# Kernel optimization log

Hardware: AMD Instinct MI355X
Metric: run time of the kernel (lower is better)

## Reference

```python
import jax, jax.numpy as jnp
import numpy as np

N_NODES = 100000
MAX_CHILD = 8
X_SIZE = 128
H_SIZE = 128
N_TYPES = 8
W_SCALE = 0.05  # keep gates out of saturation


def setup_inputs() -> dict:
    key = jax.random.key(0)
    ks = jax.random.split(key, 8)
    return {
        "x": jax.random.normal(ks[0], (N_NODES, X_SIZE), jnp.float32),
        "n_h": jax.random.normal(ks[1], (N_NODES, MAX_CHILD, H_SIZE), jnp.float32),
        "n_c": jax.random.normal(ks[2], (N_NODES, MAX_CHILD, H_SIZE), jnp.float32),
        "type_id": jax.random.randint(ks[3], (N_NODES,), 0, N_TYPES, jnp.int64),
        "W_iou": jax.random.normal(ks[4], (N_TYPES, X_SIZE, 3 * H_SIZE), jnp.float32) * W_SCALE,
        "U_iou": jax.random.normal(ks[5], (N_TYPES, H_SIZE, 3 * H_SIZE), jnp.float32) * W_SCALE,
        "b_iou": jnp.zeros((N_TYPES, 3 * H_SIZE), jnp.float32),
        "U_f": jax.random.normal(ks[6], (N_TYPES, H_SIZE, H_SIZE), jnp.float32) * W_SCALE,
        "b_f": jnp.zeros((N_TYPES, H_SIZE), jnp.float32),
    }


def reference(x, n_h, n_c, type_id, W_iou, U_iou, b_iou, U_f, b_f):
    # x: [N, X], n_h/n_c: [N, K, H] child mailbox, type_id: [N]
    N, K, H = n_h.shape
    T = W_iou.shape[0]
    h_sum = n_h.sum(axis=1)  # child-sum is linear -> aggregate before GEMM [N, H]

    # --- reduce_func: masked per-type child aggregation ---
    iou_aggr = jnp.zeros((N, 3 * H), x.dtype)
    c_aggr = jnp.zeros((N, H), x.dtype)
    for t in range(T):
        m = (type_id == t)[:, None]
        iou_t = h_sum @ U_iou[t]                                   # [N, 3H]
        f = jax.nn.sigmoid(jnp.einsum("nkh,hg->nkg", n_h, U_f[t]) + b_f[t])
        c_t = (f * n_c).sum(axis=1)                                # [N, H]
        iou_aggr = jnp.where(m, iou_t, iou_aggr)
        c_aggr = jnp.where(m, c_t, c_aggr)

    # --- apply_node_func: masked per-type node states ---
    h_out = jnp.zeros((N, H), x.dtype)
    c_out = jnp.zeros((N, H), x.dtype)
    for t in range(T):
        m = (type_id == t)[:, None]
        iou = x @ W_iou[t] + iou_aggr + b_iou[t]                   # [N, 3H]
        i_g, o_g, u_g = jnp.split(iou, 3, axis=1)
        c_t = jax.nn.sigmoid(i_g) * jnp.tanh(u_g) + c_aggr
        h_t = jax.nn.sigmoid(o_g) * jnp.tanh(c_t)
        h_out = jnp.where(m, h_t, h_out)
        c_out = jnp.where(m, c_t, c_out)
    return h_out, c_out
```

## Files before the change

kernel.cpp:

```cpp
#include <hip/hip_runtime.h>
#include <hip/hip_bf16.h>
#include <stdint.h>

typedef __bf16 bf16x8 __attribute__((ext_vector_type(8)));
typedef float  f32x4  __attribute__((ext_vector_type(4)));

#define H    128
#define KCH  8
#define NT   8
#define BM   32

#define WS_TILET  2048
#define WS_IDX    16384
#define WS_UF     458752
#define WS_W      720896

__device__ __forceinline__ float fsigm(float v){ return 1.f/(1.f+__expf(-v)); }
__device__ __forceinline__ float ftanh(float v){
  v = fminf(fmaxf(v,-15.f),15.f);
  float e = __expf(2.f*v);
  return (e-1.f)/(e+1.f);
}

__global__ void k_init(int* ws){ if (threadIdx.x < 40) ws[threadIdx.x] = 0; }

__global__ void k_detect(const int* __restrict__ type_id, int* ws){
  __shared__ int nz;
  if (threadIdx.x == 0) nz = 0;
  __syncthreads();
  int v = type_id[threadIdx.x];
  if ((threadIdx.x & 1) && v != 0) atomicAdd(&nz, 1);
  __syncthreads();
  if (threadIdx.x == 0) ws[25] = (nz == 0) ? 2 : 1;
}

__global__ void k_count(const int* __restrict__ type_id, int* __restrict__ ws, int N){
  __shared__ int h[NT];
  int tid = threadIdx.x;
  if (tid < NT) h[tid] = 0;
  __syncthreads();
  int stride = ws[25];
  int i = blockIdx.x*blockDim.x + tid;
  if (i < N) atomicAdd(&h[type_id[(size_t)i*stride]], 1);
  __syncthreads();
  if (tid < NT) atomicAdd(&ws[tid], h[tid]);
}

__global__ void k_scan(int* m){
  int s = 0;
  for (int t=0;t<NT;++t){
    m[16+t] = s;
    m[8+t]  = s;
    m[26+t] = s + m[t];
    s += ((m[t]+BM-1)/BM)*BM;
  }
  m[24] = s;
}

__global__ void k_scatter(const int* __restrict__ type_id, int* __restrict__ ws, int N){
  __shared__ int h[NT], base[NT];
  int tid = threadIdx.x;
  if (tid < NT) h[tid] = 0;
  __syncthreads();
  int stride = ws[25];
  int i = blockIdx.x*blockDim.x + tid;
  int t = 0, lp = 0;
  if (i < N){ t = type_id[(size_t)i*stride]; lp = atomicAdd(&h[t], 1); }
  __syncthreads();
  if (tid < NT) base[tid] = atomicAdd(&ws[8+tid], h[tid]);
  __syncthreads();
  if (i < N) ws[(WS_IDX/4) + base[t] + lp] = i;
}

__global__ void k_tiletype(int* ws, int ntiles){
  int i = blockIdx.x*256 + threadIdx.x;
  if (i >= ntiles) return;
  const int* op = ws + 16;
  int p = i*BM, t = -1;
  if (p < op[8]){
    for (int s=0;s<NT;++s) if (p >= op[s] && p < op[s+1]) t = s;
  }
  ws[(WS_TILET/4) + i] = t;
}

__global__ void k_prep_uf(const float* __restrict__ U_f, char* __restrict__ ws){
  int gid = blockIdx.x*256 + threadIdx.x;
  if (gid >= NT*128*16) return;
  int sp = gid & 15, c = (gid>>4) & 127, t = gid >> 11;
  int kbase = 8*(sp ^ (c & 7));
  const float* src = U_f + ((size_t)t*H + kbase)*H + c;
  bf16x8 v;
  #pragma unroll
  for (int j=0;j<8;++j) v[j] = (__bf16)src[(size_t)j*H];
  *(bf16x8*)(ws + WS_UF + (size_t)gid*16) = v;
}

__global__ void k_prep_w(const float* __restrict__ W_iou, const float* __restrict__ U_iou,
                         char* __restrict__ ws){
  int gid = blockIdx.x*256 + threadIdx.x;
  if (gid >= NT*384*32) return;
  int sp = gid & 31, col = (gid>>5) % 384, t = gid / (384*32);
  int K0 = sp*8;
  bf16x8 v;
  #pragma unroll
  for (int j=0;j<8;++j){
    int K = K0 + j;
    float f = (K < H) ? W_iou[((size_t)t*H + K)*(3*H) + col]
                      : U_iou[((size_t)t*H + (K-H))*(3*H) + col];
    v[j] = (__bf16)f;
  }
  *(bf16x8*)(ws + WS_W + (size_t)gid*16) = v;
}

__global__ __launch_bounds__(256,3) void k_phaseB(
  const float* __restrict__ n_h, const float* __restrict__ n_c,
  const float* __restrict__ b_f, const char* __restrict__ ws,
  float* __restrict__ out, int N)
{
  __shared__ __align__(16) char lds[49152];
  const int* meta = (const int*)ws;
  int tile = blockIdx.x;
  int t = ((const int*)(ws + WS_TILET))[tile];
  if (t < 0) return;
  int ev = meta[26 + t];
  const int* idx = (const int*)(ws + WS_IDX);

  int tid = threadIdx.x;
  int lane = tid & 63, wave = tid >> 6;
  int rw = wave & 1, cw = wave >> 1;
  int l15 = lane & 15, l4 = lane >> 4;
  int base = tile*BM;

  int mrow = tid >> 3, mcol = (tid & 7) * 16;
  int mpos = base + mrow;
  int mnode = (mpos < ev) ? idx[mpos] : 0;

  int npos = base + rw*16 + l15;
  bool valn = npos < ev;
  int nd = valn ? idx[npos] : 0;
  const float* ncb = n_c + (size_t)nd*(KCH*H);
  int ocb[4]; f32x4 bf4[4];
  #pragma unroll
  for (int st=0; st<4; ++st){
    ocb[st] = cw*64 + st*16 + 4*l4;
    bf4[st] = *(const f32x4*)(b_f + t*H + ocb[st]);
  }

  {
    const char* src = ws + WS_UF + (size_t)t*32768;
    #pragma unroll
    for (int it=0; it<8; ++it){
      bf16x8 v = *(const bf16x8*)(src + it*4096 + tid*16);
      *(bf16x8*)(lds + it*4096 + tid*16) = v;
    }
  }

  const float* nh_base = n_h + (size_t)mnode*(KCH*H) + mcol;

  float hsum[16];
  #pragma unroll
  for (int j=0;j<16;++j) hsum[j] = 0.f;
  f32x4 cacc[4];
  #pragma unroll
  for (int st=0;st<4;++st) cacc[st] = (f32x4){0.f,0.f,0.f,0.f};

  int arow = rw*16 + l15;
  int aswz = (arow & 7) << 4;
  int mswz = (mrow & 7) << 4;

  {
    const float4* p = (const float4*)nh_base;
    float4 a0=p[0], a1=p[1], a2=p[2], a3=p[3];
    hsum[0]+=a0.x;  hsum[1]+=a0.y;  hsum[2]+=a0.z;  hsum[3]+=a0.w;
    hsum[4]+=a1.x;  hsum[5]+=a1.y;  hsum[6]+=a1.z;  hsum[7]+=a1.w;
    hsum[8]+=a2.x;  hsum[9]+=a2.y;  hsum[10]+=a2.z; hsum[11]+=a2.w;
    hsum[12]+=a3.x; hsum[13]+=a3.y; hsum[14]+=a3.z; hsum[15]+=a3.w;
    bf16x8 w0, w1;
    w0[0]=(__bf16)a0.x; w0[1]=(__bf16)a0.y; w0[2]=(__bf16)a0.z; w0[3]=(__bf16)a0.w;
    w0[4]=(__bf16)a1.x; w0[5]=(__bf16)a1.y; w0[6]=(__bf16)a1.z; w0[7]=(__bf16)a1.w;
    w1[0]=(__bf16)a2.x; w1[1]=(__bf16)a2.y; w1[2]=(__bf16)a2.z; w1[3]=(__bf16)a2.w;
    w1[4]=(__bf16)a3.x; w1[5]=(__bf16)a3.y; w1[6]=(__bf16)a3.z; w1[7]=(__bf16)a3.w;
    *(bf16x8*)(lds + 32768 + mrow*256 + (( mcol*2      ) ^ mswz)) = w0;
    *(bf16x8*)(lds + 32768 + mrow*256 + (( mcol*2 + 16 ) ^ mswz)) = w1;
  }
  __syncthreads();

  #pragma unroll 1
  for (int k=0;k<KCH;++k){
    const int cur = 32768 + (k&1)*8192;
    const int nxt = 32768 + ((k+1)&1)*8192;
    float4 b0,b1,b2,b3;
    if (k < KCH-1){
      const float4* p = (const float4*)(nh_base + (size_t)(k+1)*H);
      b0=p[0]; b1=p[1]; b2=p[2]; b3=p[3];
    }
    f32x4 nc4[4];
    #pragma unroll
    for (int st=0;st<4;++st) nc4[st] = *(const f32x4*)(ncb + (size_t)k*H + ocb[st]);

    f32x4 fa[4];
    #pragma unroll
    for (int st=0;st<4;++st) fa[st] = (f32x4){0.f,0.f,0.f,0.f};
    #pragma unroll
    for (int kk=0; kk<4; ++kk){
      int kb = kk*64 + l4*16;
      bf16x8 bnh = *(const bf16x8*)(lds + cur + arow*256 + (kb ^ aswz));
      #pragma unroll
      for (int st=0;st<4;++st){
        int c = cw*64 + st*16 + l15;
        bf16x8 auf = *(const bf16x8*)(lds + c*256 + (kb ^ ((c&7)<<4)));
        fa[st] = __builtin_amdgcn_mfma_f32_16x16x32_bf16(auf, bnh, fa[st], 0,0,0);
      }
    }
    #pragma unroll
    for (int st=0;st<4;++st){
      #pragma unroll
      for (int r=0;r<4;++r){
        float fg = fsigm(fa[st][r] + bf4[st][r]);
        cacc[st][r] += fg * nc4[st][r];
      }
    }

    if (k < KCH-1){
      hsum[0]+=b0.x;  hsum[1]+=b0.y;  hsum[2]+=b0.z;  hsum[3]+=b0.w;
      hsum[4]+=b1.x;  hsum[5]+=b1.y;  hsum[6]+=b1.z;  hsum[7]+=b1.w;
      hsum[8]+=b2.x;  hsum[9]+=b2.y;  hsum[10]+=b2.z; hsum[11]+=b2.w;
      hsum[12]+=b3.x; hsum[13]+=b3.y; hsum[14]+=b3.z; hsum[15]+=b3.w;
      bf16x8 w0, w1;
      w0[0]=(__bf16)b0.x; w0[1]=(__bf16)b0.y; w0[2]=(__bf16)b0.z; w0[3]=(__bf16)b0.w;
      w0[4]=(__bf16)b1.x; w0[5]=(__bf16)b1.y; w0[6]=(__bf16)b1.z; w0[7]=(__bf16)b1.w;
      w1[0]=(__bf16)b2.x; w1[1]=(__bf16)b2.y; w1[2]=(__bf16)b2.z; w1[3]=(__bf16)b2.w;
      w1[4]=(__bf16)b3.x; w1[5]=(__bf16)b3.y; w1[6]=(__bf16)b3.z; w1[7]=(__bf16)b3.w;
      *(bf16x8*)(lds + nxt + mrow*256 + (( mcol*2      ) ^ mswz)) = w0;
      *(bf16x8*)(lds + nxt + mrow*256 + (( mcol*2 + 16 ) ^ mswz)) = w1;
    }
    __syncthreads();
  }

  if (mpos < ev){
    float4* dst = (float4*)(out + (size_t)mnode*H + mcol);
    dst[0] = make_float4(hsum[0], hsum[1], hsum[2], hsum[3]);
    dst[1] = make_float4(hsum[4], hsum[5], hsum[6], hsum[7]);
    dst[2] = make_float4(hsum[8], hsum[9], hsum[10],hsum[11]);
    dst[3] = make_float4(hsum[12],hsum[13],hsum[14],hsum[15]);
  }
  float* outc = out + (size_t)N*H;
  if (valn){
    #pragma unroll
    for (int st=0;st<4;++st)
      *(f32x4*)(outc + (size_t)nd*H + ocb[st]) = cacc[st];
  }
}

__global__ __launch_bounds__(256,4) void k_phaseA(
  const float* __restrict__ x, const float* __restrict__ b_iou,
  const char* __restrict__ ws, float* __restrict__ out, int N)
{
  __shared__ __align__(16) char lds[16384];
  const int* meta = (const int*)ws;
  int tile = blockIdx.x;
  int t = ((const int*)(ws + WS_TILET))[tile];
  if (t < 0) return;
  int ev = meta[26 + t];
  const int* idx = (const int*)(ws + WS_IDX);

  int tid = threadIdx.x;
  int lane = tid & 63, wave = tid >> 6;
  int rw = wave & 1, cw = wave >> 1;
  int l15 = lane & 15, l4 = lane >> 4;
  int base = tile*BM;

  int mrow = tid >> 3, mcol = (tid & 7) * 16;
  int mpos = base + mrow;
  int mnode = (mpos < ev) ? idx[mpos] : 0;

  int npos = base + rw*16 + l15;
  bool valn = npos < ev;
  int nd = valn ? idx[npos] : 0;

  int mswz = (mrow & 7) << 4;
  {
    const float4* px = (const float4*)(x   + (size_t)mnode*H + mcol);
    const float4* ph = (const float4*)(out + (size_t)mnode*H + mcol);
    float4 x0=px[0], x1=px[1], x2=px[2], x3=px[3];
    float4 h0=ph[0], h1=ph[1], h2=ph[2], h3=ph[3];
    bf16x8 w0,w1,w2,w3;
    w0[0]=(__bf16)x0.x; w0[1]=(__bf16)x0.y; w0[2]=(__bf16)x0.z; w0[3]=(__bf16)x0.w;
    w0[4]=(__bf16)x1.x; w0[5]=(__bf16)x1.y; w0[6]=(__bf16)x1.z; w0[7]=(__bf16)x1.w;
    w1[0]=(__bf16)x2.x; w1[1]=(__bf16)x2.y; w1[2]=(__bf16)x2.z; w1[3]=(__bf16)x2.w;
    w1[4]=(__bf16)x3.x; w1[5]=(__bf16)x3.y; w1[6]=(__bf16)x3.z; w1[7]=(__bf16)x3.w;
    w2[0]=(__bf16)h0.x; w2[1]=(__bf16)h0.y; w2[2]=(__bf16)h0.z; w2[3]=(__bf16)h0.w;
    w2[4]=(__bf16)h1.x; w2[5]=(__bf16)h1.y; w2[6]=(__bf16)h1.z; w2[7]=(__bf16)h1.w;
    w3[0]=(__bf16)h2.x; w3[1]=(__bf16)h2.y; w3[2]=(__bf16)h2.z; w3[3]=(__bf16)h2.w;
    w3[4]=(__bf16)h3.x; w3[5]=(__bf16)h3.y; w3[6]=(__bf16)h3.z; w3[7]=(__bf16)h3.w;
    int ab = mrow*512;
    *(bf16x8*)(lds + ab + (( mcol*2            ) ^ mswz)) = w0;
    *(bf16x8*)(lds + ab + (( mcol*2 + 16       ) ^ mswz)) = w1;
    *(bf16x8*)(lds + ab + (( 256 + mcol*2      ) ^ mswz)) = w2;
    *(bf16x8*)(lds + ab + (( 256 + mcol*2 + 16 ) ^ mswz)) = w3;
  }
  __syncthreads();

  int arow = rw*16 + l15;
  int aswz = (arow & 7) << 4;
  float* outc = out + (size_t)N*H;
  const char* wbase = ws + WS_W + (size_t)t*(384*256*2);

  #pragma unroll
  for (int st=0; st<4; ++st){
    int ocb = cw*64 + st*16 + 4*l4;
    f32x4 ag[3];
    #pragma unroll
    for (int g=0;g<3;++g) ag[g] = (f32x4){0.f,0.f,0.f,0.f};
    const char* wrow = wbase + (size_t)(cw*64 + st*16 + l15)*512;
    #pragma unroll 2
    for (int kc=0;kc<4;++kc){
      #pragma unroll
      for (int kk2=0;kk2<2;++kk2){
        int kb = kc*128 + kk2*64 + l4*16;
        bf16x8 bact = *(const bf16x8*)(lds + arow*512 + (kb ^ aswz));
        #pragma unroll
        for (int g=0;g<3;++g){
          bf16x8 aW = *(const bf16x8*)(wrow + (size_t)(g*128)*512 + kb);
          ag[g] = __builtin_amdgcn_mfma_f32_16x16x32_bf16(aW, bact, ag[g], 0,0,0);
        }
      }
    }
    if (valn){
      f32x4 bi4 = *(const f32x4*)(b_iou + t*(3*H) +        ocb);
      f32x4 bo4 = *(const f32x4*)(b_iou + t*(3*H) + H   +  ocb);
      f32x4 bu4 = *(const f32x4*)(b_iou + t*(3*H) + 2*H +  ocb);
      f32x4 ca  = *(const f32x4*)(outc + (size_t)nd*H + ocb);
      f32x4 hv4, cv4;
      #pragma unroll
      for (int r=0;r<4;++r){
        float ig = ag[0][r] + bi4[r];
        float og = ag[1][r] + bo4[r];
        float ug = ag[2][r] + bu4[r];
        float cv = fsigm(ig)*ftanh(ug) + ca[r];
        float hv = fsigm(og)*ftanh(cv);
        cv4[r] = cv; hv4[r] = hv;
      }
      *(f32x4*)(out  + (size_t)nd*H + ocb) = hv4;
      *(f32x4*)(outc + (size_t)nd*H + ocb) = cv4;
    }
  }
}

extern "C" void kernel_launch(void* const* d_in, const int* in_sizes, int n_in,
                              void* d_out, int out_size, void* d_ws, size_t ws_size,
                              hipStream_t stream){
  const float* x      = (const float*)d_in[0];
  const float* n_h    = (const float*)d_in[1];
  const float* n_c    = (const float*)d_in[2];
  const int*   typ    = (const int*)d_in[3];
  const float* W_iou  = (const float*)d_in[4];
  const float* U_iou  = (const float*)d_in[5];
  const float* b_iou  = (const float*)d_in[6];
  const float* U_f    = (const float*)d_in[7];
  const float* b_f    = (const float*)d_in[8];
  float* out = (float*)d_out;
  int*   ws  = (int*)d_ws;
  char*  wsc = (char*)d_ws;
  int N = in_sizes[0] / H;
  int nb = (N + 255) / 256;
  int ntiles = (N + NT*(BM-1) + BM-1) / BM;

  hipLaunchKernelGGL(k_init,     dim3(1),   dim3(64),  0, stream, ws);
  hipLaunchKernelGGL(k_detect,   dim3(1),   dim3(256), 0, stream, typ, ws);
  hipLaunchKernelGGL(k_count,    dim3(nb),  dim3(256), 0, stream, typ, ws, N);
  hipLaunchKernelGGL(k_scan,     dim3(1),   dim3(1),   0, stream, ws);
  hipLaunchKernelGGL(k_scatter,  dim3(nb),  dim3(256), 0, stream, typ, ws, N);
  hipLaunchKernelGGL(k_tiletype, dim3((ntiles+255)/256), dim3(256), 0, stream, ws, ntiles);
  hipLaunchKernelGGL(k_prep_uf,  dim3((NT*128*16+255)/256), dim3(256), 0, stream, U_f, wsc);
  hipLaunchKernelGGL(k_prep_w,   dim3((NT*384*32+255)/256), dim3(256), 0, stream, W_iou, U_iou, wsc);
  hipLaunchKernelGGL(k_phaseB,   dim3(ntiles), dim3(256), 0, stream,
                     n_h, n_c, b_f, wsc, out, N);
  hipLaunchKernelGGL(k_phaseA,   dim3(ntiles), dim3(256), 0, stream,
                     x, b_iou, wsc, out, N);
}
```

Measured before the change: 416.5 us.

## Fuse child-aggregation and node-apply kernels into one per-tile kernel

Merges phase B (child forget-gate GEMM and h-sum) and phase A (iou GEMM and gates) into a single kernel. The h-sum and c-aggregate stay in registers and LDS instead of being written to the output buffer and read back. This removes one launch and an intermediate round trip through global memory. In exchange, the fused kernel carries both phases' register and LDS footprint, which may lower occupancy.

```diff
diff --git a/kernel.cpp b/kernel.cpp
--- a/kernel.cpp
+++ b/kernel.cpp
@@ -112,10 +112,10 @@
   *(bf16x8*)(ws + WS_W + (size_t)gid*16) = v;
 }
 
-__global__ __launch_bounds__(256,3) void k_phaseB(
-  const float* __restrict__ n_h, const float* __restrict__ n_c,
-  const float* __restrict__ b_f, const char* __restrict__ ws,
-  float* __restrict__ out, int N)
+__global__ __launch_bounds__(256,3) void k_fused(
+  const float* __restrict__ x, const float* __restrict__ n_h, const float* __restrict__ n_c,
+  const float* __restrict__ b_iou, const float* __restrict__ b_f,
+  const char* __restrict__ ws, float* __restrict__ out, int N)
 {
   __shared__ __align__(16) char lds[49152];
   const int* meta = (const int*)ws;
@@ -237,63 +237,17 @@
     __syncthreads();
   }
 
-  if (mpos < ev){
-    float4* dst = (float4*)(out + (size_t)mnode*H + mcol);
-    dst[0] = make_float4(hsum[0], hsum[1], hsum[2], hsum[3]);
-    dst[1] = make_float4(hsum[4], hsum[5], hsum[6], hsum[7]);
-    dst[2] = make_float4(hsum[8], hsum[9], hsum[10],hsum[11]);
-    dst[3] = make_float4(hsum[12],hsum[13],hsum[14],hsum[15]);
-  }
-  float* outc = out + (size_t)N*H;
-  if (valn){
-    #pragma unroll
-    for (int st=0;st<4;++st)
-      *(f32x4*)(outc + (size_t)nd*H + ocb[st]) = cacc[st];
-  }
-}
-
-__global__ __launch_bounds__(256,4) void k_phaseA(
-  const float* __restrict__ x, const float* __restrict__ b_iou,
-  const char* __restrict__ ws, float* __restrict__ out, int N)
-{
-  __shared__ __align__(16) char lds[16384];
-  const int* meta = (const int*)ws;
-  int tile = blockIdx.x;
-  int t = ((const int*)(ws + WS_TILET))[tile];
-  if (t < 0) return;
-  int ev = meta[26 + t];
-  const int* idx = (const int*)(ws + WS_IDX);
-
-  int tid = threadIdx.x;
-  int lane = tid & 63, wave = tid >> 6;
-  int rw = wave & 1, cw = wave >> 1;
-  int l15 = lane & 15, l4 = lane >> 4;
-  int base = tile*BM;
-
-  int mrow = tid >> 3, mcol = (tid & 7) * 16;
-  int mpos = base + mrow;
-  int mnode = (mpos < ev) ? idx[mpos] : 0;
-
-  int npos = base + rw*16 + l15;
-  bool valn = npos < ev;
-  int nd = valn ? idx[npos] : 0;
-
-  int mswz = (mrow & 7) << 4;
   {
-    const float4* px = (const float4*)(x   + (size_t)mnode*H + mcol);
-    const float4* ph = (const float4*)(out + (size_t)mnode*H + mcol);
+    const float4* px = (const float4*)(x + (size_t)mnode*H + mcol);
     float4 x0=px[0], x1=px[1], x2=px[2], x3=px[3];
-    float4 h0=ph[0], h1=ph[1], h2=ph[2], h3=ph[3];
     bf16x8 w0,w1,w2,w3;
     w0[0]=(__bf16)x0.x; w0[1]=(__bf16)x0.y; w0[2]=(__bf16)x0.z; w0[3]=(__bf16)x0.w;
     w0[4]=(__bf16)x1.x; w0[5]=(__bf16)x1.y; w0[6]=(__bf16)x1.z; w0[7]=(__bf16)x1.w;
     w1[0]=(__bf16)x2.x; w1[1]=(__bf16)x2.y; w1[2]=(__bf16)x2.z; w1[3]=(__bf16)x2.w;
     w1[4]=(__bf16)x3.x; w1[5]=(__bf16)x3.y; w1[6]=(__bf16)x3.z; w1[7]=(__bf16)x3.w;
-    w2[0]=(__bf16)h0.x; w2[1]=(__bf16)h0.y; w2[2]=(__bf16)h0.z; w2[3]=(__bf16)h0.w;
-    w2[4]=(__bf16)h1.x; w2[5]=(__bf16)h1.y; w2[6]=(__bf16)h1.z; w2[7]=(__bf16)h1.w;
-    w3[0]=(__bf16)h2.x; w3[1]=(__bf16)h2.y; w3[2]=(__bf16)h2.z; w3[3]=(__bf16)h2.w;
-    w3[4]=(__bf16)h3.x; w3[5]=(__bf16)h3.y; w3[6]=(__bf16)h3.z; w3[7]=(__bf16)h3.w;
-    int ab = mrow*512;
+    #pragma unroll
+    for (int j=0;j<8;++j){ w2[j]=(__bf16)hsum[j]; w3[j]=(__bf16)hsum[8+j]; }
+    int ab = 32768 + mrow*512;
     *(bf16x8*)(lds + ab + (( mcol*2            ) ^ mswz)) = w0;
     *(bf16x8*)(lds + ab + (( mcol*2 + 16       ) ^ mswz)) = w1;
     *(bf16x8*)(lds + ab + (( 256 + mcol*2      ) ^ mswz)) = w2;
@@ -301,14 +255,9 @@
   }
   __syncthreads();
 
-  int arow = rw*16 + l15;
-  int aswz = (arow & 7) << 4;
-  float* outc = out + (size_t)N*H;
   const char* wbase = ws + WS_W + (size_t)t*(384*256*2);
-
   #pragma unroll
   for (int st=0; st<4; ++st){
-    int ocb = cw*64 + st*16 + 4*l4;
     f32x4 ag[3];
     #pragma unroll
     for (int g=0;g<3;++g) ag[g] = (f32x4){0.f,0.f,0.f,0.f};
@@ -318,7 +267,7 @@
       #pragma unroll
       for (int kk2=0;kk2<2;++kk2){
         int kb = kc*128 + kk2*64 + l4*16;
-        bf16x8 bact = *(const bf16x8*)(lds + arow*512 + (kb ^ aswz));
+        bf16x8 bact = *(const bf16x8*)(lds + 32768 + arow*512 + (kb ^ aswz));
         #pragma unroll
         for (int g=0;g<3;++g){
           bf16x8 aW = *(const bf16x8*)(wrow + (size_t)(g*128)*512 + kb);
@@ -327,22 +276,21 @@
       }
     }
     if (valn){
-      f32x4 bi4 = *(const f32x4*)(b_iou + t*(3*H) +        ocb);
-      f32x4 bo4 = *(const f32x4*)(b_iou + t*(3*H) + H   +  ocb);
-      f32x4 bu4 = *(const f32x4*)(b_iou + t*(3*H) + 2*H +  ocb);
-      f32x4 ca  = *(const f32x4*)(outc + (size_t)nd*H + ocb);
+      f32x4 bi4 = *(const f32x4*)(b_iou + t*(3*H) +        ocb[st]);
+      f32x4 bo4 = *(const f32x4*)(b_iou + t*(3*H) + H   +  ocb[st]);
+      f32x4 bu4 = *(const f32x4*)(b_iou + t*(3*H) + 2*H +  ocb[st]);
       f32x4 hv4, cv4;
       #pragma unroll
       for (int r=0;r<4;++r){
         float ig = ag[0][r] + bi4[r];
         float og = ag[1][r] + bo4[r];
         float ug = ag[2][r] + bu4[r];
-        float cv = fsigm(ig)*ftanh(ug) + ca[r];
+        float cv = fsigm(ig)*ftanh(ug) + cacc[st][r];
         float hv = fsigm(og)*ftanh(cv);
         cv4[r] = cv; hv4[r] = hv;
       }
-      *(f32x4*)(out  + (size_t)nd*H + ocb) = hv4;
-      *(f32x4*)(outc + (size_t)nd*H + ocb) = cv4;
+      *(f32x4*)(out + (size_t)nd*H + ocb[st]) = hv4;
+      *(f32x4*)(out + (size_t)N*H + (size_t)nd*H + ocb[st]) = cv4;
     }
   }
 }
@@ -374,8 +322,6 @@
   hipLaunchKernelGGL(k_tiletype, dim3((ntiles+255)/256), dim3(256), 0, stream, ws, ntiles);
   hipLaunchKernelGGL(k_prep_uf,  dim3((NT*128*16+255)/256), dim3(256), 0, stream, U_f, wsc);
   hipLaunchKernelGGL(k_prep_w,   dim3((NT*384*32+255)/256), dim3(256), 0, stream, W_iou, U_iou, wsc);
-  hipLaunchKernelGGL(k_phaseB,   dim3(ntiles), dim3(256), 0, stream,
-                     n_h, n_c, b_f, wsc, out, N);
-  hipLaunchKernelGGL(k_phaseA,   dim3(ntiles), dim3(256), 0, stream,
-                     x, b_iou, wsc, out, N);
-}
+  hipLaunchKernelGGL(k_fused,    dim3(ntiles), dim3(256), 0, stream,
+                     x, n_h, n_c, b_iou, b_f, wsc, out, N);
+}
```

Result: faster. 362.4 us (-13.0%).
